# Kernel optimization log

Measured on AMD Instinct MI355X. Metric: run time of the kernel, lower is better.

Reference implementation:

```python
import jax, jax.numpy as jnp
import numpy as np

N_NODES = 100000
N_EDGES = 1600000
IN_F = 256
OUT_F = 128
KEEP_P = 0.5  # dropout p = 0.5 -> keep prob 0.5, scale 1/keep


def setup_inputs() -> dict:
    key = jax.random.key(0)
    k_x, k_w, k_v, k_m, k_r, k_c = jax.random.split(key, 6)
    x = jax.random.normal(k_x, (N_NODES, IN_F), dtype=jnp.float32)
    # reset_parameters: uniform(-stdv, stdv), stdv = sqrt(6/(in+out))
    stdv = float(np.sqrt(6.0 / (IN_F + OUT_F)))
    weight = jax.random.uniform(k_w, (IN_F, OUT_F), dtype=jnp.float32,
                                minval=-stdv, maxval=stdv)
    adj_val = jax.random.uniform(k_v, (N_EDGES,), dtype=jnp.float32)
    # deterministic dropout mask: bernoulli(keep)/keep -> values in {0, 2}
    drop_mask = (jax.random.bernoulli(k_m, KEEP_P, (N_NODES, IN_F))
                 .astype(jnp.float32) / KEEP_P)
    edge_row = jax.random.randint(k_r, (N_EDGES,), 0, N_NODES, dtype=jnp.int32)
    edge_col = jax.random.randint(k_c, (N_EDGES,), 0, N_NODES, dtype=jnp.int32)
    return {"input": x, "weight": weight, "adj_val": adj_val,
            "drop_mask": drop_mask, "edge_row": edge_row, "edge_col": edge_col}


def reference(input, weight, adj_val, drop_mask, edge_row, edge_col):
    # dropout (deterministic mask) -> dense matmul
    x = (input * drop_mask) @ weight                      # [N, OUT_F]
    # spmm(adj, x): out[i] = sum_{e: row[e]==i} val[e] * x[col[e]]
    msgs = adj_val[:, None] * x[edge_col]                 # [E, OUT_F]
    out = jax.ops.segment_sum(msgs, edge_row, num_segments=N_NODES)
    return jax.nn.relu(out)
```

## Files before the change

kernel.cpp:

```cpp
#include <hip/hip_runtime.h>

#define IN_F 256
#define OUT_F 128
#define RWB 196
#define CAPL 48
#define BCAP 4096
#define EPBA 4096

typedef __attribute__((ext_vector_type(8))) short short8v;
typedef __attribute__((ext_vector_type(4))) float float4v;

__device__ inline unsigned short f2bf(float f) {
    unsigned u = __float_as_uint(f);
    u += 0x7fff + ((u >> 16) & 1);
    return (unsigned short)(u >> 16);
}

__global__ __launch_bounds__(512)
__attribute__((amdgpu_waves_per_eu(4, 8)))
void gemm_mfma_kernel(const float* __restrict__ in,
                      const float* __restrict__ mask,
                      const float* __restrict__ W,
                      unsigned short* __restrict__ xb, int N) {
    __shared__ __align__(128) char A2[32768];
    const int tid  = threadIdx.x;
    const int lane = tid & 63;
    const int w    = tid >> 6;
    const int l15  = lane & 15;
    const int q    = lane >> 4;

    short8v bfrag[8];
    {
        const int col = w * 16 + l15;
#pragma unroll
        for (int s = 0; s < 8; ++s) {
            int k0 = s * 32 + q * 8;
            short8v b;
#pragma unroll
            for (int j = 0; j < 8; ++j)
                b[j] = (short)f2bf(W[(size_t)(k0 + j) * OUT_F + col]);
            bfrag[s] = b;
        }
    }

    const int srow = tid >> 4;
    const int skc2 = (tid & 15) * 32;
    const int sxr  = (srow & 7) << 4;
    const int axr  = (l15 & 7) << 4;

    const int ntiles = (N + 31) >> 5;
    int tile = blockIdx.x;
    if (tile >= ntiles) return;

    const float4* in4 = (const float4*)in;
    const float4* mk4 = (const float4*)mask;

    float4 pin[4], pmk[4];
    {
        int grow = tile * 32 + srow;
        size_t base = (size_t)grow * 64 + (skc2 >> 3);
#pragma unroll
        for (int j = 0; j < 4; ++j) {
            if (grow < N) { pin[j] = in4[base + j]; pmk[j] = mk4[base + j]; }
            else { pin[j] = make_float4(0.f,0.f,0.f,0.f); pmk[j] = make_float4(0.f,0.f,0.f,0.f); }
        }
    }
    int cur = 0;

    for (; tile < ntiles; tile += gridDim.x) {
        {
            float f[16];
#pragma unroll
            for (int j = 0; j < 4; ++j) {
                f[j*4+0] = pin[j].x * pmk[j].x;
                f[j*4+1] = pin[j].y * pmk[j].y;
                f[j*4+2] = pin[j].z * pmk[j].z;
                f[j*4+3] = pin[j].w * pmk[j].w;
            }
            short8v h0, h1;
#pragma unroll
            for (int j = 0; j < 8; ++j) {
                h0[j] = (short)f2bf(f[j]);
                h1[j] = (short)f2bf(f[8 + j]);
            }
            char* Bb = A2 + cur * 16384;
            *(short8v*)(Bb + srow * 512 + (skc2 ^ sxr))        = h0;
            *(short8v*)(Bb + srow * 512 + ((skc2 + 16) ^ sxr)) = h1;
        }

        int nt = tile + gridDim.x;
        if (nt < ntiles) {
            int grow = nt * 32 + srow;
            size_t base = (size_t)grow * 64 + (skc2 >> 3);
#pragma unroll
            for (int j = 0; j < 4; ++j) {
                if (grow < N) { pin[j] = in4[base + j]; pmk[j] = mk4[base + j]; }
                else { pin[j] = make_float4(0.f,0.f,0.f,0.f); pmk[j] = make_float4(0.f,0.f,0.f,0.f); }
            }
        }

        __syncthreads();

        float4v acc0 = {0.f, 0.f, 0.f, 0.f};
        float4v acc1 = {0.f, 0.f, 0.f, 0.f};
        const char* Ab = A2 + cur * 16384;
#pragma unroll
        for (int s = 0; s < 8; ++s) {
            int so = (s * 64 + q * 16) ^ axr;
            short8v a0 = *(const short8v*)(Ab + l15 * 512 + so);
            short8v a1 = *(const short8v*)(Ab + (16 + l15) * 512 + so);
            acc0 = __builtin_amdgcn_mfma_f32_16x16x32_bf16(a0, bfrag[s], acc0, 0, 0, 0);
            acc1 = __builtin_amdgcn_mfma_f32_16x16x32_bf16(a1, bfrag[s], acc1, 0, 0, 0);
        }

        int gcol = w * 16 + l15;
        int gr0  = tile * 32 + q * 4;
#pragma unroll
        for (int r = 0; r < 4; ++r) {
            int grow = gr0 + r;
            if (grow < N) xb[(size_t)grow * OUT_F + gcol] = f2bf(acc0[r]);
        }
        int gr1 = gr0 + 16;
#pragma unroll
        for (int r = 0; r < 4; ++r) {
            int grow = gr1 + r;
            if (grow < N) xb[(size_t)grow * OUT_F + gcol] = f2bf(acc1[r]);
        }

        cur ^= 1;
    }
}

__global__ __launch_bounds__(512)
void partition_kernel(const int* __restrict__ edge_row,
                      const int* __restrict__ edge_col,
                      const float* __restrict__ adj_val,
                      int* __restrict__ g_bcnt,
                      uint2* __restrict__ g_edges, int E) {
    __shared__ int bcnt[512], scan[512], curs[512], bbase[512];
    __shared__ uint2 stage[EPBA];
    __shared__ int tgt[EPBA];
    const int tid = threadIdx.x;
    const int e0  = blockIdx.x * EPBA;

    bcnt[tid] = 0;
    __syncthreads();

#pragma unroll
    for (int j = 0; j < EPBA / 512; ++j) {
        int e = e0 + j * 512 + tid;
        if (e < E) atomicAdd(&bcnt[edge_row[e] / RWB], 1);
    }
    __syncthreads();

    int v = bcnt[tid];
    scan[tid] = v;
    __syncthreads();
    for (int d = 1; d < 512; d <<= 1) {
        int t = (tid >= d) ? scan[tid - d] : 0;
        __syncthreads();
        scan[tid] += t;
        __syncthreads();
    }
    bbase[tid] = (v > 0) ? atomicAdd(&g_bcnt[tid], v) : 0;
    curs[tid]  = scan[tid] - v;
    __syncthreads();

#pragma unroll
    for (int j = 0; j < EPBA / 512; ++j) {
        int e = e0 + j * 512 + tid;
        if (e < E) {
            int r  = edge_row[e];
            int b  = r / RWB;
            int rl = r - b * RWB;
            unsigned u = __float_as_uint(adj_val[e]);
            u += 0xFFFFu + ((u >> 17) & 1);
            int pos = atomicAdd(&curs[b], 1);
            uint2 p;
            p.x = ((unsigned)edge_col[e] << 15) | (u >> 17);
            p.y = (unsigned)rl;
            stage[pos] = p;
            int inb = bbase[b] + (pos - (scan[b] - bcnt[b]));
            tgt[pos] = (inb < BCAP) ? (b * BCAP + inb) : -1;
        }
    }
    __syncthreads();

    int total = min(EPBA, E - e0);
    for (int i = tid; i < total; i += 512) {
        int t = tgt[i];
        if (t >= 0) g_edges[t] = stage[i];
    }
}

__global__ __launch_bounds__(512)
void bucket_gather_kernel(const unsigned short* __restrict__ xb,
                          const uint2* __restrict__ g_edges,
                          const int* __restrict__ g_bcnt,
                          float* __restrict__ out, int N) {
    __shared__ int lcnt[RWB];
    __shared__ unsigned lcv[RWB * CAPL];
    const int tid = threadIdx.x;
    const int b   = blockIdx.x;

    for (int i = tid; i < RWB; i += 512) lcnt[i] = 0;
    __syncthreads();

    int n = g_bcnt[b];
    if (n > BCAP) n = BCAP;
    const uint2* src = g_edges + (size_t)b * BCAP;
    for (int i = tid; i < n; i += 512) {
        uint2 e = src[i];
        int rl = (int)e.y;
        int pos = atomicAdd(&lcnt[rl], 1);
        if (pos < CAPL) lcv[rl * CAPL + pos] = e.x;
    }
    __syncthreads();

    const uint4* xq = (const uint4*)xb;
    const int lane = tid & 15;
    const int sub  = tid >> 4;
    const int r0   = b * RWB;
    for (int base = 0; base < RWB; base += 32) {
        int rl = base + sub;
        int g  = r0 + rl;
        if (rl < RWB && g < N) {
            int e1 = lcnt[rl];
            if (e1 > CAPL) e1 = CAPL;
            const unsigned* bucket = &lcv[rl * CAPL];
            float acc[8] = {0.f,0.f,0.f,0.f,0.f,0.f,0.f,0.f};
            int e = 0;
            for (; e + 1 < e1; e += 2) {
                unsigned c0 = bucket[e];
                unsigned c1 = bucket[e + 1];
                uint4 a = xq[(size_t)(c0 >> 15) * 16 + lane];
                uint4 bb = xq[(size_t)(c1 >> 15) * 16 + lane];
                float v0 = __uint_as_float((c0 & 0x7FFFu) << 17);
                float v1 = __uint_as_float((c1 & 0x7FFFu) << 17);
                acc[0] += v0 * __uint_as_float(a.x << 16);
                acc[1] += v0 * __uint_as_float(a.x & 0xffff0000u);
                acc[2] += v0 * __uint_as_float(a.y << 16);
                acc[3] += v0 * __uint_as_float(a.y & 0xffff0000u);
                acc[4] += v0 * __uint_as_float(a.z << 16);
                acc[5] += v0 * __uint_as_float(a.z & 0xffff0000u);
                acc[6] += v0 * __uint_as_float(a.w << 16);
                acc[7] += v0 * __uint_as_float(a.w & 0xffff0000u);
                acc[0] += v1 * __uint_as_float(bb.x << 16);
                acc[1] += v1 * __uint_as_float(bb.x & 0xffff0000u);
                acc[2] += v1 * __uint_as_float(bb.y << 16);
                acc[3] += v1 * __uint_as_float(bb.y & 0xffff0000u);
                acc[4] += v1 * __uint_as_float(bb.z << 16);
                acc[5] += v1 * __uint_as_float(bb.z & 0xffff0000u);
                acc[6] += v1 * __uint_as_float(bb.w << 16);
                acc[7] += v1 * __uint_as_float(bb.w & 0xffff0000u);
            }
            if (e < e1) {
                unsigned c0 = bucket[e];
                uint4 a = xq[(size_t)(c0 >> 15) * 16 + lane];
                float v = __uint_as_float((c0 & 0x7FFFu) << 17);
                acc[0] += v * __uint_as_float(a.x << 16);
                acc[1] += v * __uint_as_float(a.x & 0xffff0000u);
                acc[2] += v * __uint_as_float(a.y << 16);
                acc[3] += v * __uint_as_float(a.y & 0xffff0000u);
                acc[4] += v * __uint_as_float(a.z << 16);
                acc[5] += v * __uint_as_float(a.z & 0xffff0000u);
                acc[6] += v * __uint_as_float(a.w << 16);
                acc[7] += v * __uint_as_float(a.w & 0xffff0000u);
            }
            float4 o0, o1;
            o0.x = fmaxf(acc[0], 0.f); o0.y = fmaxf(acc[1], 0.f);
            o0.z = fmaxf(acc[2], 0.f); o0.w = fmaxf(acc[3], 0.f);
            o1.x = fmaxf(acc[4], 0.f); o1.y = fmaxf(acc[5], 0.f);
            o1.z = fmaxf(acc[6], 0.f); o1.w = fmaxf(acc[7], 0.f);
            float4* dst = (float4*)(out + (size_t)g * OUT_F + lane * 8);
            dst[0] = o0;
            dst[1] = o1;
        }
    }
}

static inline size_t align_up(size_t v, size_t a) { return (v + a - 1) & ~(a - 1); }

extern "C" void kernel_launch(void* const* d_in, const int* in_sizes, int n_in,
                              void* d_out, int out_size, void* d_ws, size_t ws_size,
                              hipStream_t stream) {
    const float* input     = (const float*)d_in[0];
    const float* weight    = (const float*)d_in[1];
    const float* adj_val   = (const float*)d_in[2];
    const float* drop_mask = (const float*)d_in[3];
    const int*   edge_row  = (const int*)d_in[4];
    const int*   edge_col  = (const int*)d_in[5];
    float* out = (float*)d_out;

    const int N = in_sizes[0] / IN_F;
    const int E = in_sizes[2];
    const int NB = (N + RWB - 1) / RWB;
    const int nblkA = (E + EPBA - 1) / EPBA;

    char* ws = (char*)d_ws;
    size_t off = 0;
    unsigned short* xbf = (unsigned short*)(ws + off);
    off = align_up(off + (size_t)N * OUT_F * 2, 256);
    int* g_bcnt = (int*)(ws + off);          off = align_up(off + 512 * 4, 256);
    uint2* g_edges = (uint2*)(ws + off);     off = align_up(off + (size_t)NB * BCAP * 8, 256);

    gemm_mfma_kernel<<<512, 512, 0, stream>>>(input, drop_mask, weight, xbf, N);

    hipMemsetAsync(g_bcnt, 0, 512 * 4, stream);
    partition_kernel<<<nblkA, 512, 0, stream>>>(edge_row, edge_col, adj_val,
                                                g_bcnt, g_edges, E);

    bucket_gather_kernel<<<NB, 512, 0, stream>>>(xbf, g_edges, g_bcnt, out, N);
}
```

Baseline: 148.3 us.

## Launch one GEMM block per tile and fold counter reset into GEMM

The GEMM kernel no longer runs a persistent grid-stride loop with double-buffered LDS and register prefetch. It now launches one block per 32-row tile, which is about 3125 blocks, and issues the input loads before the weight-fragment loads so both are in flight together. The separate hipMemsetAsync that cleared the bucket counters is removed, and block 0 of the GEMM zeroes them instead, which saves one stream operation. In exchange, every block reloads and converts the full weight slice, so weight traffic grows by about six times. The cross-tile prefetch overlap is also lost, and occupancy now has to hide latency instead.

```diff
diff --git a/kernel.cpp b/kernel.cpp
--- a/kernel.cpp
+++ b/kernel.cpp
@@ -21,40 +21,25 @@
 void gemm_mfma_kernel(const float* __restrict__ in,
                       const float* __restrict__ mask,
                       const float* __restrict__ W,
-                      unsigned short* __restrict__ xb, int N) {
-    __shared__ __align__(128) char A2[32768];
+                      unsigned short* __restrict__ xb, int N,
+                      int* __restrict__ g_bcnt) {
+    __shared__ __align__(128) char A2[16384];
     const int tid  = threadIdx.x;
     const int lane = tid & 63;
     const int w    = tid >> 6;
     const int l15  = lane & 15;
     const int q    = lane >> 4;
 
-    short8v bfrag[8];
-    {
-        const int col = w * 16 + l15;
-#pragma unroll
-        for (int s = 0; s < 8; ++s) {
-            int k0 = s * 32 + q * 8;
-            short8v b;
-#pragma unroll
-            for (int j = 0; j < 8; ++j)
-                b[j] = (short)f2bf(W[(size_t)(k0 + j) * OUT_F + col]);
-            bfrag[s] = b;
-        }
-    }
+    if (blockIdx.x == 0) g_bcnt[tid] = 0;
+
+    const int tile = blockIdx.x;
+    const int ntiles = (N + 31) >> 5;
+    if (tile >= ntiles) return;
 
     const int srow = tid >> 4;
     const int skc2 = (tid & 15) * 32;
-    const int sxr  = (srow & 7) << 4;
-    const int axr  = (l15 & 7) << 4;
-
-    const int ntiles = (N + 31) >> 5;
-    int tile = blockIdx.x;
-    if (tile >= ntiles) return;
-
     const float4* in4 = (const float4*)in;
     const float4* mk4 = (const float4*)mask;
-
     float4 pin[4], pmk[4];
     {
         int grow = tile * 32 + srow;
@@ -65,69 +50,67 @@
             else { pin[j] = make_float4(0.f,0.f,0.f,0.f); pmk[j] = make_float4(0.f,0.f,0.f,0.f); }
         }
     }
-    int cur = 0;
-
-    for (; tile < ntiles; tile += gridDim.x) {
-        {
-            float f[16];
-#pragma unroll
-            for (int j = 0; j < 4; ++j) {
-                f[j*4+0] = pin[j].x * pmk[j].x;
-                f[j*4+1] = pin[j].y * pmk[j].y;
-                f[j*4+2] = pin[j].z * pmk[j].z;
-                f[j*4+3] = pin[j].w * pmk[j].w;
-            }
-            short8v h0, h1;
-#pragma unroll
-            for (int j = 0; j < 8; ++j) {
-                h0[j] = (short)f2bf(f[j]);
-                h1[j] = (short)f2bf(f[8 + j]);
-            }
-            char* Bb = A2 + cur * 16384;
-            *(short8v*)(Bb + srow * 512 + (skc2 ^ sxr))        = h0;
-            *(short8v*)(Bb + srow * 512 + ((skc2 + 16) ^ sxr)) = h1;
-        }
-
-        int nt = tile + gridDim.x;
-        if (nt < ntiles) {
-            int grow = nt * 32 + srow;
-            size_t base = (size_t)grow * 64 + (skc2 >> 3);
-#pragma unroll
-            for (int j = 0; j < 4; ++j) {
-                if (grow < N) { pin[j] = in4[base + j]; pmk[j] = mk4[base + j]; }
-                else { pin[j] = make_float4(0.f,0.f,0.f,0.f); pmk[j] = make_float4(0.f,0.f,0.f,0.f); }
-            }
-        }
-
-        __syncthreads();
-
-        float4v acc0 = {0.f, 0.f, 0.f, 0.f};
-        float4v acc1 = {0.f, 0.f, 0.f, 0.f};
-        const char* Ab = A2 + cur * 16384;
+
+    short8v bfrag[8];
+    {
+        const int col = w * 16 + l15;
 #pragma unroll
         for (int s = 0; s < 8; ++s) {
-            int so = (s * 64 + q * 16) ^ axr;
-            short8v a0 = *(const short8v*)(Ab + l15 * 512 + so);
-            short8v a1 = *(const short8v*)(Ab + (16 + l15) * 512 + so);
-            acc0 = __builtin_amdgcn_mfma_f32_16x16x32_bf16(a0, bfrag[s], acc0, 0, 0, 0);
-            acc1 = __builtin_amdgcn_mfma_f32_16x16x32_bf16(a1, bfrag[s], acc1, 0, 0, 0);
-        }
-
-        int gcol = w * 16 + l15;
-        int gr0  = tile * 32 + q * 4;
-#pragma unroll
-        for (int r = 0; r < 4; ++r) {
-            int grow = gr0 + r;
-            if (grow < N) xb[(size_t)grow * OUT_F + gcol] = f2bf(acc0[r]);
-        }
-        int gr1 = gr0 + 16;
-#pragma unroll
-        for (int r = 0; r < 4; ++r) {
-            int grow = gr1 + r;
-            if (grow < N) xb[(size_t)grow * OUT_F + gcol] = f2bf(acc1[r]);
-        }
-
-        cur ^= 1;
+            int k0 = s * 32 + q * 8;
+            short8v b;
+#pragma unroll
+            for (int j = 0; j < 8; ++j)
+                b[j] = (short)f2bf(W[(size_t)(k0 + j) * OUT_F + col]);
+            bfrag[s] = b;
+        }
+    }
+
+    const int sxr = (srow & 7) << 4;
+    {
+        float f[16];
+#pragma unroll
+        for (int j = 0; j < 4; ++j) {
+            f[j*4+0] = pin[j].x * pmk[j].x;
+            f[j*4+1] = pin[j].y * pmk[j].y;
+            f[j*4+2] = pin[j].z * pmk[j].z;
+            f[j*4+3] = pin[j].w * pmk[j].w;
+        }
+        short8v h0, h1;
+#pragma unroll
+        for (int j = 0; j < 8; ++j) {
+            h0[j] = (short)f2bf(f[j]);
+            h1[j] = (short)f2bf(f[8 + j]);
+        }
+        *(short8v*)(A2 + srow * 512 + (skc2 ^ sxr))        = h0;
+        *(short8v*)(A2 + srow * 512 + ((skc2 + 16) ^ sxr)) = h1;
+    }
+
+    __syncthreads();
+
+    const int axr = (l15 & 7) << 4;
+    float4v acc0 = {0.f, 0.f, 0.f, 0.f};
+    float4v acc1 = {0.f, 0.f, 0.f, 0.f};
+#pragma unroll
+    for (int s = 0; s < 8; ++s) {
+        int so = (s * 64 + q * 16) ^ axr;
+        short8v a0 = *(const short8v*)(A2 + l15 * 512 + so);
+        short8v a1 = *(const short8v*)(A2 + (16 + l15) * 512 + so);
+        acc0 = __builtin_amdgcn_mfma_f32_16x16x32_bf16(a0, bfrag[s], acc0, 0, 0, 0);
+        acc1 = __builtin_amdgcn_mfma_f32_16x16x32_bf16(a1, bfrag[s], acc1, 0, 0, 0);
+    }
+
+    int gcol = w * 16 + l15;
+    int gr0  = tile * 32 + q * 4;
+#pragma unroll
+    for (int r = 0; r < 4; ++r) {
+        int grow = gr0 + r;
+        if (grow < N) xb[(size_t)grow * OUT_F + gcol] = f2bf(acc0[r]);
+    }
+    int gr1 = gr0 + 16;
+#pragma unroll
+    for (int r = 0; r < 4; ++r) {
+        int grow = gr1 + r;
+        if (grow < N) xb[(size_t)grow * OUT_F + gcol] = f2bf(acc1[r]);
     }
 }
 
@@ -296,6 +279,7 @@
     const int E = in_sizes[2];
     const int NB = (N + RWB - 1) / RWB;
     const int nblkA = (E + EPBA - 1) / EPBA;
+    const int ntiles = (N + 31) / 32;
 
     char* ws = (char*)d_ws;
     size_t off = 0;
@@ -304,9 +288,9 @@
     int* g_bcnt = (int*)(ws + off);          off = align_up(off + 512 * 4, 256);
     uint2* g_edges = (uint2*)(ws + off);     off = align_up(off + (size_t)NB * BCAP * 8, 256);
 
-    gemm_mfma_kernel<<<512, 512, 0, stream>>>(input, drop_mask, weight, xbf, N);
-
-    hipMemsetAsync(g_bcnt, 0, 512 * 4, stream);
+    gemm_mfma_kernel<<<ntiles, 512, 0, stream>>>(input, drop_mask, weight,
+                                                 xbf, N, g_bcnt);
+
     partition_kernel<<<nblkA, 512, 0, stream>>>(edge_row, edge_col, adj_val,
                                                 g_bcnt, g_edges, E);
 
```

After: 158.8 us. 7.1% more time.
